# Kernel tuning notes

Measured on AMD Instinct MI355X. Metric: run time of the kernel, lower is better.

The kernel has to match this reference:

```python
import jax, jax.numpy as jnp
import numpy as np

N_EMBD = 384
HEAD_SIZE = 16

def setup_inputs() -> dict:
    key = jax.random.key(0)
    k1, k2, k3, k4 = jax.random.split(key, 4)
    B, T = 4, 4096
    x = jax.random.normal(k1, (B, T, N_EMBD), dtype=jnp.float32)
    # nn.Linear(n_embd, head_size, bias=False): y = x @ W^T, W: [head_size, n_embd].
    # Store transposed [n_embd, head_size] for direct matmul.
    s = 1.0 / np.sqrt(N_EMBD)
    Wk = jax.random.uniform(k2, (N_EMBD, HEAD_SIZE), jnp.float32, -s, s)
    Wq = jax.random.uniform(k3, (N_EMBD, HEAD_SIZE), jnp.float32, -s, s)
    Wv = jax.random.uniform(k4, (N_EMBD, HEAD_SIZE), jnp.float32, -s, s)
    return {"x": x, "Wk": Wk, "Wq": Wq, "Wv": Wv}

def reference(x, Wk, Wq, Wv):
    B, T, C = x.shape
    k = x @ Wk  # [B,T,H]
    q = x @ Wq
    v = x @ Wv
    scale = k.shape[-1] ** -0.5
    wei = jnp.einsum('bth,bsh->bts', q, k) * scale  # [B,T,T]
    causal = jnp.tril(jnp.ones((T, T), dtype=bool))
    wei = jnp.where(causal, wei, -jnp.inf)
    wei = jax.nn.softmax(wei, axis=-1)
    out = jnp.einsum('bts,bsh->bth', wei, v)  # [B,T,H]
    return out
```

## Files before the change

kernel.cpp:

```cpp
#include <hip/hip_runtime.h>
#include <hip/hip_bf16.h>


constexpr int B_DIM = 4;
constexpr int T_SEQ = 4096;
constexpr int C_DIM = 384;
constexpr int H_DIM = 16;
constexpr int NROW  = B_DIM * T_SEQ;

typedef __bf16 bf16x8 __attribute__((ext_vector_type(8)));
typedef float  f32x4  __attribute__((ext_vector_type(4)));

__device__ __forceinline__ unsigned short f2bf(float f) {
  unsigned int u = __builtin_bit_cast(unsigned int, f);
  u += 0x7fffu + ((u >> 16) & 1u);
  return (unsigned short)(u >> 16);
}
__device__ __forceinline__ bf16x8 as_bf16x8(uint4 u) {
  return __builtin_bit_cast(bf16x8, u);
}
__device__ __forceinline__ unsigned pk2(float a, float b) {
  float2 t; t.x = a; t.y = b;
  __hip_bfloat162 h = __float22bfloat162_rn(t);
  unsigned u;
  __builtin_memcpy(&u, &h, 4);
  return u;
}

__global__ __launch_bounds__(256) void wconv(
    const float* __restrict__ Wk, const float* __restrict__ Wq,
    const float* __restrict__ Wv, unsigned short* __restrict__ WT) {
  const int i = blockIdx.x * 256 + threadIdx.x;
  const int m = i / 6144;
  const int r = i - m * 6144;
  const int n = r / 384;
  const int k = r - n * 384;
  const float* __restrict__ W = (m == 0) ? Wk : (m == 1) ? Wq : Wv;
  WT[i] = f2bf(W[k * 16 + n]);
}

__global__ __launch_bounds__(128) void qkv_mfma(
    const float* __restrict__ x, const unsigned short* __restrict__ WT,
    unsigned short* __restrict__ Kb,
    unsigned short* __restrict__ Qb,
    unsigned short* __restrict__ VTb)
{
  const int tid  = threadIdx.x;
  const int w    = tid >> 6;
  const int lane = tid & 63;
  const int quad = lane >> 4;
  const int col  = lane & 15;
  const int r0   = blockIdx.x << 4;
  const int kb   = w * 6;

  __shared__ float mrg[12][64];

  const float4* __restrict__ xp =
      reinterpret_cast<const float4*>(x + (size_t)(r0 + col) * C_DIM) + quad * 2;
  float4 araw[12];
#pragma unroll
  for (int kk = 0; kk < 6; ++kk) {
    araw[2 * kk]     = xp[(kb + kk) * 8];
    araw[2 * kk + 1] = xp[(kb + kk) * 8 + 1];
  }

  const uint4* __restrict__ bk = reinterpret_cast<const uint4*>(
      WT + (size_t)col * 384 + quad * 8);
  const uint4* __restrict__ bq = bk + 768;
  const uint4* __restrict__ bv = bk + 1536;

  f32x4 ck = {0.f, 0.f, 0.f, 0.f};
  f32x4 cq = {0.f, 0.f, 0.f, 0.f};
  f32x4 cv = {0.f, 0.f, 0.f, 0.f};
#pragma unroll
  for (int kk = 0; kk < 6; ++kk) {
    uint4 pk;
    const float4 a0 = araw[2 * kk], a1 = araw[2 * kk + 1];
    pk.x = pk2(a0.x, a0.y);
    pk.y = pk2(a0.z, a0.w);
    pk.z = pk2(a1.x, a1.y);
    pk.w = pk2(a1.z, a1.w);
    const bf16x8 av = as_bf16x8(pk);
    ck = __builtin_amdgcn_mfma_f32_16x16x32_bf16(av, as_bf16x8(bk[(kb + kk) * 4]), ck, 0, 0, 0);
    cq = __builtin_amdgcn_mfma_f32_16x16x32_bf16(av, as_bf16x8(bq[(kb + kk) * 4]), cq, 0, 0, 0);
    cv = __builtin_amdgcn_mfma_f32_16x16x32_bf16(av, as_bf16x8(bv[(kb + kk) * 4]), cv, 0, 0, 0);
  }

  if (w == 1) {
#pragma unroll
    for (int r = 0; r < 4; ++r) {
      mrg[r][lane]     = ck[r];
      mrg[4 + r][lane] = cq[r];
      mrg[8 + r][lane] = cv[r];
    }
  }
  __syncthreads();
  if (w == 0) {
    const float SC = 0.25f * 1.44269504088896341f;
#pragma unroll
    for (int r = 0; r < 4; ++r) {
      const float vk = ck[r] + mrg[r][lane];
      const float vq = cq[r] + mrg[4 + r][lane];
      const float vv = cv[r] + mrg[8 + r][lane];
      const int row = r0 + quad * 4 + r;
      Kb[row * 16 + col]      = f2bf(vk);
      Qb[row * 32 + col]      = f2bf(vq * SC);
      Qb[row * 32 + 16 + col] = 0;
      const int bb = row >> 12, t = row & 4095;
      VTb[(((size_t)(bb * 16 + col)) << 12) + t] = f2bf(vv);
    }
  }
}

__global__ __launch_bounds__(256, 8) void flash_v6(
    const unsigned short* __restrict__ Qb,
    const unsigned short* __restrict__ Kb,
    const unsigned short* __restrict__ VTb,
    float* __restrict__ PO, float* __restrict__ PL)
{
  const int tid  = threadIdx.x;
  const int w    = tid >> 6;
  const int lane = tid & 63;
  const int quad = lane >> 4;
  const int col  = lane & 15;
  const int qt   = 255 - (blockIdx.x >> 3);
  const int b    = (blockIdx.x >> 1) & 3;
  const int h2   = blockIdx.x & 1;
  const int slot = h2 * 4 + w;
  const int r0   = qt << 4;

  const bf16x8 qb = as_bf16x8(*reinterpret_cast<const uint4*>(
      Qb + (((size_t)(b * T_SEQ + r0 + col)) << 5) + quad * 8));

  f32x4 o = {0.f, 0.f, 0.f, 0.f};
  float l = 0.f;

  const unsigned short* Kbase = Kb + ((size_t)(b * T_SEQ) << 4);
  const unsigned short* Vrow  = VTb + (((size_t)(b * 16 + col)) << 12);
  const int nch = (qt + 4) >> 2;

  for (int c = slot; c < nch; c += 8) {
    const int kt0 = c << 2;
    const bool diag = (kt0 + 4 > qt);

#pragma unroll
    for (int i = 0; i < 2; ++i) {
      const int vbase = kt0 * 16 + i * 32 + quad * 4;
      const uint2 v0 = *reinterpret_cast<const uint2*>(Vrow + vbase);
      const uint2 v1 = *reinterpret_cast<const uint2*>(Vrow + vbase + 16);

      float p[2][4];
#pragma unroll
      for (int t2 = 0; t2 < 2; ++t2) {
        const int kt = kt0 + 2 * i + t2;
        const uint4 kf = *reinterpret_cast<const uint4*>(
            Kbase + (((size_t)(kt * 16 + col)) << 4) + quad * 8);
        f32x4 z = {0.f, 0.f, 0.f, 0.f};
        f32x4 s = __builtin_amdgcn_mfma_f32_16x16x32_bf16(
            as_bf16x8(kf), qb, z, 0, 0, 0);
        if (diag) {
          const int kb0 = kt * 16 + quad * 4 - r0;
#pragma unroll
          for (int r = 0; r < 4; ++r)
            if (kb0 + r > col) s[r] = -1e30f;
        }
#pragma unroll
        for (int r = 0; r < 4; ++r) {
          p[t2][r] = __builtin_amdgcn_exp2f(s[r]);
          l += p[t2][r];
        }
      }

      uint4 pb;
      pb.x = pk2(p[0][0], p[0][1]);
      pb.y = pk2(p[0][2], p[0][3]);
      pb.z = pk2(p[1][0], p[1][1]);
      pb.w = pk2(p[1][2], p[1][3]);
      const uint4 va = make_uint4(v0.x, v0.y, v1.x, v1.y);
      o = __builtin_amdgcn_mfma_f32_16x16x32_bf16(
          as_bf16x8(va), as_bf16x8(pb), o, 0, 0, 0);
    }
  }

  l += __shfl_xor(l, 16);
  l += __shfl_xor(l, 32);

  const size_t rowbase = (size_t)b * T_SEQ + r0;
  float* pO = PO + ((size_t)slot * NROW + rowbase) * 16;
  *reinterpret_cast<float4*>(pO + col * 16 + quad * 4) =
      __builtin_bit_cast(float4, o);
  if (quad == 0) PL[(size_t)slot * NROW + rowbase + col] = l;
}

__global__ __launch_bounds__(256) void flash_merge(
    const float* __restrict__ PO, const float* __restrict__ PL,
    float* __restrict__ out)
{
  const int i   = blockIdx.x * 256 + threadIdx.x;
  const int row = i >> 4;
  float O = 0.f, L = 0.f;
#pragma unroll
  for (int s = 0; s < 8; ++s) {
    O += PO[((size_t)s * NROW) * 16 + i];
    L += PL[(size_t)s * NROW + row];
  }
  out[i] = O / L;
}

extern "C" void kernel_launch(void* const* d_in, const int* in_sizes, int n_in,
                              void* d_out, int out_size, void* d_ws, size_t ws_size,
                              hipStream_t stream) {
  const float* x  = (const float*)d_in[0];
  const float* Wk = (const float*)d_in[1];
  const float* Wq = (const float*)d_in[2];
  const float* Wv = (const float*)d_in[3];
  float* outp = (float*)d_out;

  unsigned short* Qb  = (unsigned short*)d_ws;
  unsigned short* Kb  = Qb + (size_t)NROW * 32;
  unsigned short* VTb = Kb + (size_t)NROW * 16 + 64;
  unsigned short* WT  = VTb + (size_t)NROW * 16;
  float* PO = (float*)(WT + 18432);
  float* PL = PO + (size_t)8 * NROW * 16;

  wconv<<<72, 256, 0, stream>>>(Wk, Wq, Wv, WT);
  qkv_mfma<<<1024, 128, 0, stream>>>(x, WT, Kb, Qb, VTb);
  flash_v6<<<2048, 256, 0, stream>>>(Qb, Kb, VTb, PO, PL);
  flash_merge<<<1024, 256, 0, stream>>>(PO, PL, outp);
}
```

Baseline: 106.6 us.

## Fuse weight conversion, QKV projection, attention and merge into one cooperative kernel

Replaces four kernel launches with a single cooperative kernel that uses grid-wide syncs between the weight conversion, QKV projection and flash-attention phases. The attention split-K partials are now reduced in shared memory within a block instead of being written to global memory and merged by a separate kernel. Query tiles are paired so each block processes balanced causal work. The trade-offs are grid sync costs, halved parallelism in the attention phase, and a requirement that all 1024 blocks be co-resident.

```diff
diff --git a/kernel.cpp b/kernel.cpp
--- a/kernel.cpp
+++ b/kernel.cpp
@@ -1,5 +1,8 @@
 #include <hip/hip_runtime.h>
 #include <hip/hip_bf16.h>
+#include <hip/hip_cooperative_groups.h>
+
+namespace cg = cooperative_groups;
 
 
 constexpr int B_DIM = 4;
@@ -27,184 +30,191 @@
   return u;
 }
 
-__global__ __launch_bounds__(256) void wconv(
+__global__ __launch_bounds__(256, 4) void fused_head(
+    const float* __restrict__ x,
     const float* __restrict__ Wk, const float* __restrict__ Wq,
-    const float* __restrict__ Wv, unsigned short* __restrict__ WT) {
-  const int i = blockIdx.x * 256 + threadIdx.x;
-  const int m = i / 6144;
-  const int r = i - m * 6144;
-  const int n = r / 384;
-  const int k = r - n * 384;
-  const float* __restrict__ W = (m == 0) ? Wk : (m == 1) ? Wq : Wv;
-  WT[i] = f2bf(W[k * 16 + n]);
-}
-
-__global__ __launch_bounds__(128) void qkv_mfma(
-    const float* __restrict__ x, const unsigned short* __restrict__ WT,
+    const float* __restrict__ Wv,
     unsigned short* __restrict__ Kb,
     unsigned short* __restrict__ Qb,
-    unsigned short* __restrict__ VTb)
+    unsigned short* __restrict__ VTb,
+    unsigned short* __restrict__ WT,
+    float* __restrict__ out)
 {
+  __shared__ float smem[2304];
   const int tid  = threadIdx.x;
   const int w    = tid >> 6;
   const int lane = tid & 63;
   const int quad = lane >> 4;
   const int col  = lane & 15;
-  const int r0   = blockIdx.x << 4;
-  const int kb   = w * 6;
-
-  __shared__ float mrg[12][64];
-
-  const float4* __restrict__ xp =
-      reinterpret_cast<const float4*>(x + (size_t)(r0 + col) * C_DIM) + quad * 2;
-  float4 araw[12];
-#pragma unroll
-  for (int kk = 0; kk < 6; ++kk) {
-    araw[2 * kk]     = xp[(kb + kk) * 8];
-    araw[2 * kk + 1] = xp[(kb + kk) * 8 + 1];
+  const int blk  = blockIdx.x;
+  cg::grid_group grid = cg::this_grid();
+
+  {
+    const int i = blk * 256 + tid;
+    if (i < 18432) {
+      const int m = i / 6144;
+      const int r = i - m * 6144;
+      const int n = r / 384;
+      const int k = r - n * 384;
+      const float* __restrict__ W = (m == 0) ? Wk : (m == 1) ? Wq : Wv;
+      WT[i] = f2bf(W[k * 16 + n]);
+    }
   }
-
-  const uint4* __restrict__ bk = reinterpret_cast<const uint4*>(
-      WT + (size_t)col * 384 + quad * 8);
-  const uint4* __restrict__ bq = bk + 768;
-  const uint4* __restrict__ bv = bk + 1536;
-
-  f32x4 ck = {0.f, 0.f, 0.f, 0.f};
-  f32x4 cq = {0.f, 0.f, 0.f, 0.f};
-  f32x4 cv = {0.f, 0.f, 0.f, 0.f};
-#pragma unroll
-  for (int kk = 0; kk < 6; ++kk) {
-    uint4 pk;
-    const float4 a0 = araw[2 * kk], a1 = araw[2 * kk + 1];
-    pk.x = pk2(a0.x, a0.y);
-    pk.y = pk2(a0.z, a0.w);
-    pk.z = pk2(a1.x, a1.y);
-    pk.w = pk2(a1.z, a1.w);
-    const bf16x8 av = as_bf16x8(pk);
-    ck = __builtin_amdgcn_mfma_f32_16x16x32_bf16(av, as_bf16x8(bk[(kb + kk) * 4]), ck, 0, 0, 0);
-    cq = __builtin_amdgcn_mfma_f32_16x16x32_bf16(av, as_bf16x8(bq[(kb + kk) * 4]), cq, 0, 0, 0);
-    cv = __builtin_amdgcn_mfma_f32_16x16x32_bf16(av, as_bf16x8(bv[(kb + kk) * 4]), cv, 0, 0, 0);
+  grid.sync();
+
+  {
+    const int r0 = blk << 4;
+    const int kb = w * 3;
+    const float4* __restrict__ xp =
+        reinterpret_cast<const float4*>(x + (size_t)(r0 + col) * C_DIM) + quad * 2;
+    float4 araw[6];
+#pragma unroll
+    for (int kk = 0; kk < 3; ++kk) {
+      araw[2 * kk]     = xp[(kb + kk) * 8];
+      araw[2 * kk + 1] = xp[(kb + kk) * 8 + 1];
+    }
+
+    const uint4* __restrict__ bk_ = reinterpret_cast<const uint4*>(
+        WT + (size_t)col * 384 + quad * 8);
+    const uint4* __restrict__ bq_ = bk_ + 768;
+    const uint4* __restrict__ bv_ = bk_ + 1536;
+
+    f32x4 ck = {0.f, 0.f, 0.f, 0.f};
+    f32x4 cq = {0.f, 0.f, 0.f, 0.f};
+    f32x4 cv = {0.f, 0.f, 0.f, 0.f};
+#pragma unroll
+    for (int kk = 0; kk < 3; ++kk) {
+      uint4 pk;
+      const float4 a0 = araw[2 * kk], a1 = araw[2 * kk + 1];
+      pk.x = pk2(a0.x, a0.y);
+      pk.y = pk2(a0.z, a0.w);
+      pk.z = pk2(a1.x, a1.y);
+      pk.w = pk2(a1.z, a1.w);
+      const bf16x8 av = as_bf16x8(pk);
+      ck = __builtin_amdgcn_mfma_f32_16x16x32_bf16(av, as_bf16x8(bk_[(kb + kk) * 4]), ck, 0, 0, 0);
+      cq = __builtin_amdgcn_mfma_f32_16x16x32_bf16(av, as_bf16x8(bq_[(kb + kk) * 4]), cq, 0, 0, 0);
+      cv = __builtin_amdgcn_mfma_f32_16x16x32_bf16(av, as_bf16x8(bv_[(kb + kk) * 4]), cv, 0, 0, 0);
+    }
+
+    if (w != 0) {
+      float* m0 = smem + (w - 1) * 768;
+#pragma unroll
+      for (int r = 0; r < 4; ++r) {
+        m0[r * 64 + lane]        = ck[r];
+        m0[(4 + r) * 64 + lane]  = cq[r];
+        m0[(8 + r) * 64 + lane]  = cv[r];
+      }
+    }
+    __syncthreads();
+    if (w == 0) {
+      const float SC = 0.25f * 1.44269504088896341f;
+#pragma unroll
+      for (int r = 0; r < 4; ++r) {
+        float vk = ck[r], vq = cq[r], vv = cv[r];
+#pragma unroll
+        for (int w2 = 0; w2 < 3; ++w2) {
+          vk += smem[w2 * 768 + r * 64 + lane];
+          vq += smem[w2 * 768 + (4 + r) * 64 + lane];
+          vv += smem[w2 * 768 + (8 + r) * 64 + lane];
+        }
+        const int row = r0 + quad * 4 + r;
+        Kb[row * 16 + col]      = f2bf(vk);
+        Qb[row * 32 + col]      = f2bf(vq * SC);
+        Qb[row * 32 + 16 + col] = 0;
+        const int bb = row >> 12, t = row & 4095;
+        VTb[(((size_t)(bb * 16 + col)) << 12) + t] = f2bf(vv);
+      }
+    }
   }
-
-  if (w == 1) {
-#pragma unroll
-    for (int r = 0; r < 4; ++r) {
-      mrg[r][lane]     = ck[r];
-      mrg[4 + r][lane] = cq[r];
-      mrg[8 + r][lane] = cv[r];
+  grid.sync();
+
+  {
+    const int p  = blk >> 3;
+    const int h2 = (blk >> 2) & 1;
+    const int b  = blk & 3;
+    const int qt = h2 ? 255 - p : p;
+    const int r0 = qt << 4;
+
+    const bf16x8 qb = as_bf16x8(*reinterpret_cast<const uint4*>(
+        Qb + (((size_t)(b * T_SEQ + r0 + col)) << 5) + quad * 8));
+
+    f32x4 o = {0.f, 0.f, 0.f, 0.f};
+    float l = 0.f;
+
+    const unsigned short* Kbase = Kb + ((size_t)(b * T_SEQ) << 4);
+    const unsigned short* Vrow  = VTb + (((size_t)(b * 16 + col)) << 12);
+    const int nch = (qt + 4) >> 2;
+
+    for (int c = w; c < nch; c += 4) {
+      const int kt0 = c << 2;
+      const bool diag = (kt0 + 4 > qt);
+
+#pragma unroll
+      for (int i = 0; i < 2; ++i) {
+        const int vbase = kt0 * 16 + i * 32 + quad * 4;
+        const uint2 v0 = *reinterpret_cast<const uint2*>(Vrow + vbase);
+        const uint2 v1 = *reinterpret_cast<const uint2*>(Vrow + vbase + 16);
+
+        float pp[2][4];
+#pragma unroll
+        for (int t2 = 0; t2 < 2; ++t2) {
+          const int kt = kt0 + 2 * i + t2;
+          const uint4 kf = *reinterpret_cast<const uint4*>(
+              Kbase + (((size_t)(kt * 16 + col)) << 4) + quad * 8);
+          f32x4 z = {0.f, 0.f, 0.f, 0.f};
+          f32x4 s = __builtin_amdgcn_mfma_f32_16x16x32_bf16(
+              as_bf16x8(kf), qb, z, 0, 0, 0);
+          if (diag) {
+            const int kb0 = kt * 16 + quad * 4 - r0;
+#pragma unroll
+            for (int r = 0; r < 4; ++r)
+              if (kb0 + r > col) s[r] = -1e30f;
+          }
+#pragma unroll
+          for (int r = 0; r < 4; ++r) {
+            pp[t2][r] = __builtin_amdgcn_exp2f(s[r]);
+            l += pp[t2][r];
+          }
+        }
+
+        uint4 pb;
+        pb.x = pk2(pp[0][0], pp[0][1]);
+        pb.y = pk2(pp[0][2], pp[0][3]);
+        pb.z = pk2(pp[1][0], pp[1][1]);
+        pb.w = pk2(pp[1][2], pp[1][3]);
+        const uint4 va = make_uint4(v0.x, v0.y, v1.x, v1.y);
+        o = __builtin_amdgcn_mfma_f32_16x16x32_bf16(
+            as_bf16x8(va), as_bf16x8(pb), o, 0, 0, 0);
+      }
+    }
+
+    l += __shfl_xor(l, 16);
+    l += __shfl_xor(l, 32);
+
+    float* mrgO = smem;
+    float* mrgL = smem + 1024;
+#pragma unroll
+    for (int r = 0; r < 4; ++r)
+      mrgO[w * 256 + (quad * 4 + r) * 16 + col] = o[r];
+    if (quad == 0) mrgL[w * 16 + col] = l;
+    __syncthreads();
+
+    if (w == 0) {
+      const float L = mrgL[col] + mrgL[16 + col] + mrgL[32 + col] + mrgL[48 + col];
+      const float rinv = 1.0f / L;
+      float4 O;
+#pragma unroll
+      for (int r = 0; r < 4; ++r) {
+        float s = 0.f;
+#pragma unroll
+        for (int w2 = 0; w2 < 4; ++w2)
+          s += mrgO[w2 * 256 + (quad * 4 + r) * 16 + col];
+        (&O.x)[r] = s * rinv;
+      }
+      *reinterpret_cast<float4*>(
+          out + (((size_t)(b * T_SEQ + r0 + col)) << 4) + quad * 4) = O;
     }
   }
-  __syncthreads();
-  if (w == 0) {
-    const float SC = 0.25f * 1.44269504088896341f;
-#pragma unroll
-    for (int r = 0; r < 4; ++r) {
-      const float vk = ck[r] + mrg[r][lane];
-      const float vq = cq[r] + mrg[4 + r][lane];
-      const float vv = cv[r] + mrg[8 + r][lane];
-      const int row = r0 + quad * 4 + r;
-      Kb[row * 16 + col]      = f2bf(vk);
-      Qb[row * 32 + col]      = f2bf(vq * SC);
-      Qb[row * 32 + 16 + col] = 0;
-      const int bb = row >> 12, t = row & 4095;
-      VTb[(((size_t)(bb * 16 + col)) << 12) + t] = f2bf(vv);
-    }
-  }
-}
-
-__global__ __launch_bounds__(256, 8) void flash_v6(
-    const unsigned short* __restrict__ Qb,
-    const unsigned short* __restrict__ Kb,
-    const unsigned short* __restrict__ VTb,
-    float* __restrict__ PO, float* __restrict__ PL)
-{
-  const int tid  = threadIdx.x;
-  const int w    = tid >> 6;
-  const int lane = tid & 63;
-  const int quad = lane >> 4;
-  const int col  = lane & 15;
-  const int qt   = 255 - (blockIdx.x >> 3);
-  const int b    = (blockIdx.x >> 1) & 3;
-  const int h2   = blockIdx.x & 1;
-  const int slot = h2 * 4 + w;
-  const int r0   = qt << 4;
-
-  const bf16x8 qb = as_bf16x8(*reinterpret_cast<const uint4*>(
-      Qb + (((size_t)(b * T_SEQ + r0 + col)) << 5) + quad * 8));
-
-  f32x4 o = {0.f, 0.f, 0.f, 0.f};
-  float l = 0.f;
-
-  const unsigned short* Kbase = Kb + ((size_t)(b * T_SEQ) << 4);
-  const unsigned short* Vrow  = VTb + (((size_t)(b * 16 + col)) << 12);
-  const int nch = (qt + 4) >> 2;
-
-  for (int c = slot; c < nch; c += 8) {
-    const int kt0 = c << 2;
-    const bool diag = (kt0 + 4 > qt);
-
-#pragma unroll
-    for (int i = 0; i < 2; ++i) {
-      const int vbase = kt0 * 16 + i * 32 + quad * 4;
-      const uint2 v0 = *reinterpret_cast<const uint2*>(Vrow + vbase);
-      const uint2 v1 = *reinterpret_cast<const uint2*>(Vrow + vbase + 16);
-
-      float p[2][4];
-#pragma unroll
-      for (int t2 = 0; t2 < 2; ++t2) {
-        const int kt = kt0 + 2 * i + t2;
-        const uint4 kf = *reinterpret_cast<const uint4*>(
-            Kbase + (((size_t)(kt * 16 + col)) << 4) + quad * 8);
-        f32x4 z = {0.f, 0.f, 0.f, 0.f};
-        f32x4 s = __builtin_amdgcn_mfma_f32_16x16x32_bf16(
-            as_bf16x8(kf), qb, z, 0, 0, 0);
-        if (diag) {
-          const int kb0 = kt * 16 + quad * 4 - r0;
-#pragma unroll
-          for (int r = 0; r < 4; ++r)
-            if (kb0 + r > col) s[r] = -1e30f;
-        }
-#pragma unroll
-        for (int r = 0; r < 4; ++r) {
-          p[t2][r] = __builtin_amdgcn_exp2f(s[r]);
-          l += p[t2][r];
-        }
-      }
-
-      uint4 pb;
-      pb.x = pk2(p[0][0], p[0][1]);
-      pb.y = pk2(p[0][2], p[0][3]);
-      pb.z = pk2(p[1][0], p[1][1]);
-      pb.w = pk2(p[1][2], p[1][3]);
-      const uint4 va = make_uint4(v0.x, v0.y, v1.x, v1.y);
-      o = __builtin_amdgcn_mfma_f32_16x16x32_bf16(
-          as_bf16x8(va), as_bf16x8(pb), o, 0, 0, 0);
-    }
-  }
-
-  l += __shfl_xor(l, 16);
-  l += __shfl_xor(l, 32);
-
-  const size_t rowbase = (size_t)b * T_SEQ + r0;
-  float* pO = PO + ((size_t)slot * NROW + rowbase) * 16;
-  *reinterpret_cast<float4*>(pO + col * 16 + quad * 4) =
-      __builtin_bit_cast(float4, o);
-  if (quad == 0) PL[(size_t)slot * NROW + rowbase + col] = l;
-}
-
-__global__ __launch_bounds__(256) void flash_merge(
-    const float* __restrict__ PO, const float* __restrict__ PL,
-    float* __restrict__ out)
-{
-  const int i   = blockIdx.x * 256 + threadIdx.x;
-  const int row = i >> 4;
-  float O = 0.f, L = 0.f;
-#pragma unroll
-  for (int s = 0; s < 8; ++s) {
-    O += PO[((size_t)s * NROW) * 16 + i];
-    L += PL[(size_t)s * NROW + row];
-  }
-  out[i] = O / L;
 }
 
 extern "C" void kernel_launch(void* const* d_in, const int* in_sizes, int n_in,
@@ -220,11 +230,10 @@
   unsigned short* Kb  = Qb + (size_t)NROW * 32;
   unsigned short* VTb = Kb + (size_t)NROW * 16 + 64;
   unsigned short* WT  = VTb + (size_t)NROW * 16;
-  float* PO = (float*)(WT + 18432);
-  float* PL = PO + (size_t)8 * NROW * 16;
-
-  wconv<<<72, 256, 0, stream>>>(Wk, Wq, Wv, WT);
-  qkv_mfma<<<1024, 128, 0, stream>>>(x, WT, Kb, Qb, VTb);
-  flash_v6<<<2048, 256, 0, stream>>>(Qb, Kb, VTb, PO, PL);
-  flash_merge<<<1024, 256, 0, stream>>>(PO, PL, outp);
-}
+
+  void* args[] = {(void*)&x, (void*)&Wk, (void*)&Wq, (void*)&Wv,
+                  (void*)&Kb, (void*)&Qb, (void*)&VTb, (void*)&WT,
+                  (void*)&outp};
+  hipLaunchCooperativeKernel((const void*)fused_head, dim3(1024), dim3(256),
+                             args, 0, stream);
+}
```

Result: slower. 287.2 us (+169.6%).

## Fuse split-K merge into flash kernel via shared-memory reduction across four waves

Applied to the files above, without the earlier changes.

Each block now handles a full 16-row query tile with four waves splitting the key chunks, then reduces the partial outputs and softmax denominators in shared memory and writes the normalized output directly. This drops the separate merge kernel and the global round trip of the eight-way partial buffers, along with one launch. In exchange the grid halves to 1024 blocks and each wave walks twice as many chunks, which reduces parallelism for the causal workload, and the occupancy hint in the launch bounds is removed.

```diff
diff --git a/kernel.cpp b/kernel.cpp
--- a/kernel.cpp
+++ b/kernel.cpp
@@ -112,21 +112,21 @@
   }
 }
 
-__global__ __launch_bounds__(256, 8) void flash_v6(
+__global__ __launch_bounds__(256) void flash(
     const unsigned short* __restrict__ Qb,
     const unsigned short* __restrict__ Kb,
     const unsigned short* __restrict__ VTb,
-    float* __restrict__ PO, float* __restrict__ PL)
+    float* __restrict__ out)
 {
+  __shared__ float mrgO[1024];
+  __shared__ float mrgL[64];
   const int tid  = threadIdx.x;
   const int w    = tid >> 6;
   const int lane = tid & 63;
   const int quad = lane >> 4;
   const int col  = lane & 15;
-  const int qt   = 255 - (blockIdx.x >> 3);
-  const int b    = (blockIdx.x >> 1) & 3;
-  const int h2   = blockIdx.x & 1;
-  const int slot = h2 * 4 + w;
+  const int qt   = 255 - (blockIdx.x >> 2);
+  const int b    = blockIdx.x & 3;
   const int r0   = qt << 4;
 
   const bf16x8 qb = as_bf16x8(*reinterpret_cast<const uint4*>(
@@ -139,7 +139,7 @@
   const unsigned short* Vrow  = VTb + (((size_t)(b * 16 + col)) << 12);
   const int nch = (qt + 4) >> 2;
 
-  for (int c = slot; c < nch; c += 8) {
+  for (int c = w; c < nch; c += 4) {
     const int kt0 = c << 2;
     const bool diag = (kt0 + 4 > qt);
 
@@ -149,7 +149,7 @@
       const uint2 v0 = *reinterpret_cast<const uint2*>(Vrow + vbase);
       const uint2 v1 = *reinterpret_cast<const uint2*>(Vrow + vbase + 16);
 
-      float p[2][4];
+      float pp[2][4];
 #pragma unroll
       for (int t2 = 0; t2 < 2; ++t2) {
         const int kt = kt0 + 2 * i + t2;
@@ -166,16 +166,16 @@
         }
 #pragma unroll
         for (int r = 0; r < 4; ++r) {
-          p[t2][r] = __builtin_amdgcn_exp2f(s[r]);
-          l += p[t2][r];
+          pp[t2][r] = __builtin_amdgcn_exp2f(s[r]);
+          l += pp[t2][r];
         }
       }
 
       uint4 pb;
-      pb.x = pk2(p[0][0], p[0][1]);
-      pb.y = pk2(p[0][2], p[0][3]);
-      pb.z = pk2(p[1][0], p[1][1]);
-      pb.w = pk2(p[1][2], p[1][3]);
+      pb.x = pk2(pp[0][0], pp[0][1]);
+      pb.y = pk2(pp[0][2], pp[0][3]);
+      pb.z = pk2(pp[1][0], pp[1][1]);
+      pb.w = pk2(pp[1][2], pp[1][3]);
       const uint4 va = make_uint4(v0.x, v0.y, v1.x, v1.y);
       o = __builtin_amdgcn_mfma_f32_16x16x32_bf16(
           as_bf16x8(va), as_bf16x8(pb), o, 0, 0, 0);
@@ -185,26 +185,27 @@
   l += __shfl_xor(l, 16);
   l += __shfl_xor(l, 32);
 
-  const size_t rowbase = (size_t)b * T_SEQ + r0;
-  float* pO = PO + ((size_t)slot * NROW + rowbase) * 16;
-  *reinterpret_cast<float4*>(pO + col * 16 + quad * 4) =
-      __builtin_bit_cast(float4, o);
-  if (quad == 0) PL[(size_t)slot * NROW + rowbase + col] = l;
-}
-
-__global__ __launch_bounds__(256) void flash_merge(
-    const float* __restrict__ PO, const float* __restrict__ PL,
-    float* __restrict__ out)
-{
-  const int i   = blockIdx.x * 256 + threadIdx.x;
-  const int row = i >> 4;
-  float O = 0.f, L = 0.f;
-#pragma unroll
-  for (int s = 0; s < 8; ++s) {
-    O += PO[((size_t)s * NROW) * 16 + i];
-    L += PL[(size_t)s * NROW + row];
-  }
-  out[i] = O / L;
+#pragma unroll
+  for (int r = 0; r < 4; ++r)
+    mrgO[w * 256 + (quad * 4 + r) * 16 + col] = o[r];
+  if (quad == 0) mrgL[w * 16 + col] = l;
+  __syncthreads();
+
+  if (w == 0) {
+    const float L = mrgL[col] + mrgL[16 + col] + mrgL[32 + col] + mrgL[48 + col];
+    const float rinv = 1.0f / L;
+    float4 O;
+#pragma unroll
+    for (int r = 0; r < 4; ++r) {
+      float s = 0.f;
+#pragma unroll
+      for (int w2 = 0; w2 < 4; ++w2)
+        s += mrgO[w2 * 256 + (quad * 4 + r) * 16 + col];
+      (&O.x)[r] = s * rinv;
+    }
+    *reinterpret_cast<float4*>(
+        out + (((size_t)(b * T_SEQ + r0 + col)) << 4) + quad * 4) = O;
+  }
 }
 
 extern "C" void kernel_launch(void* const* d_in, const int* in_sizes, int n_in,
@@ -220,11 +221,8 @@
   unsigned short* Kb  = Qb + (size_t)NROW * 32;
   unsigned short* VTb = Kb + (size_t)NROW * 16 + 64;
   unsigned short* WT  = VTb + (size_t)NROW * 16;
-  float* PO = (float*)(WT + 18432);
-  float* PL = PO + (size_t)8 * NROW * 16;
 
   wconv<<<72, 256, 0, stream>>>(Wk, Wq, Wv, WT);
   qkv_mfma<<<1024, 128, 0, stream>>>(x, WT, Kb, Qb, VTb);
-  flash_v6<<<2048, 256, 0, stream>>>(Qb, Kb, VTb, PO, PL);
-  flash_merge<<<1024, 256, 0, stream>>>(PO, PL, outp);
-}
+  flash<<<1024, 256, 0, stream>>>(Qb, Kb, VTb, outp);
+}
```

After: 107.0 us. Within noise of the previous version (+0.4%).
